# Performance work log

Hardware: AMD Instinct MI355X
Metric: run time of the kernel (lower is better)

The kernel has to match this reference:

```python
import jax, jax.numpy as jnp
import numpy as np

EPS = 1e-5

def _bn_eval(x, gamma, beta, mu, var):
    # channelwise BN (eval mode) on [B,C,N,K]
    inv = gamma / jnp.sqrt(var + EPS)
    return x * inv[None, :, None, None] + (beta - mu * inv)[None, :, None, None]

def _gather_nk(x, idx):
    # x: [B,C,N], idx: [B,N,K] -> [B,C,N,K]
    return jnp.take_along_axis(x[:, :, None, :], idx[:, None, :, :], axis=3)

def setup_inputs() -> dict:
    key = jax.random.key(0)
    ks = jax.random.split(key, 20)
    B, N, K, C = 2, 16384, 16, 128
    s = 0.05
    inp = {
        'coord': jax.random.normal(ks[0], (B, N, 3), jnp.float32),
        'feature_spa': jax.random.normal(ks[1], (B, C, N), jnp.float32),
        'feature_spe': jax.random.normal(ks[2], (B, C, N), jnp.float32),
        'neighbor_indices': jax.random.randint(ks[3], (B, N, K), 0, N),
        'wq': jax.random.normal(ks[4], (C, C), jnp.float32) * s,
        'wk': jax.random.normal(ks[5], (C, C), jnp.float32) * s,
        'wv_w': jax.random.normal(ks[6], (C, C), jnp.float32) * s,
        'wv_b': jax.random.normal(ks[7], (C,), jnp.float32) * s,
        'pos_w1': jax.random.normal(ks[8], (3, 3), jnp.float32) * 0.3,
        'pos_b1': jax.random.normal(ks[9], (3,), jnp.float32) * 0.1,
        'pos_g': jnp.ones((3,), jnp.float32),
        'pos_beta': jnp.zeros((3,), jnp.float32),
        'pos_mu': jnp.zeros((3,), jnp.float32),
        'pos_var': jnp.ones((3,), jnp.float32),
        'pos_w2': jax.random.normal(ks[10], (1, 3), jnp.float32) * 0.3,
        'pos_b2': jax.random.normal(ks[11], (1,), jnp.float32) * 0.1,
        'sc_w1': jax.random.normal(ks[12], (2, 2), jnp.float32) * 0.3,
        'sc_b1': jax.random.normal(ks[13], (2,), jnp.float32) * 0.1,
        'sc_g': jnp.ones((2,), jnp.float32),
        'sc_beta': jnp.zeros((2,), jnp.float32),
        'sc_mu': jnp.zeros((2,), jnp.float32),
        'sc_var': jnp.ones((2,), jnp.float32),
        'sc_w2': jax.random.normal(ks[14], (1, 2), jnp.float32) * 0.3,
        'sc_b2': jax.random.normal(ks[15], (1,), jnp.float32) * 0.1,
    }
    return inp

def reference(coord, feature_spa, feature_spe, neighbor_indices,
              wq, wk, wv_w, wv_b,
              pos_w1, pos_b1, pos_g, pos_beta, pos_mu, pos_var, pos_w2, pos_b2,
              sc_w1, sc_b1, sc_g, sc_beta, sc_mu, sc_var, sc_w2, sc_b2):
    C = feature_spa.shape[1]
    coord_t = jnp.transpose(coord, (0, 2, 1))                      # [B,3,N]
    Q = jnp.einsum('oc,bcn->bon', wq, feature_spa)                 # [B,C,N]
    Kf = jnp.einsum('oc,bcn->bon', wk, feature_spe)
    V = jnp.einsum('oc,bcn->bon', wv_w, feature_spe) + wv_b[None, :, None]
    # positional branch
    neighbor_coord = _gather_nk(coord_t, neighbor_indices)         # [B,3,N,K]
    coord_diff = neighbor_coord - coord_t[:, :, :, None]
    g = jnp.exp(-2.0 * coord_diff ** 2)                            # [B,3,N,K]
    h = jnp.einsum('oc,bcnk->bonk', pos_w1, g) + pos_b1[None, :, None, None]
    h = jax.nn.relu(_bn_eval(h, pos_g, pos_beta, pos_mu, pos_var))
    scores_coord = jnp.einsum('oc,bcnk->bonk', pos_w2, h) + pos_b2[None, :, None, None]  # [B,1,N,K]
    # feature branch
    Kg = _gather_nk(Kf, neighbor_indices)                          # [B,C,N,K]
    Vg = _gather_nk(V, neighbor_indices)                           # [B,C,N,K]
    scores_feat = jnp.einsum('bcn,bcnk->bnk', Q, Kg) / np.sqrt(C)  # [B,N,K]
    scores = jnp.concatenate([scores_coord, scores_feat[:, None]], axis=1)  # [B,2,N,K]
    s = jnp.einsum('oc,bcnk->bonk', sc_w1, scores) + sc_b1[None, :, None, None]
    s = jax.nn.relu(_bn_eval(s, sc_g, sc_beta, sc_mu, sc_var))
    s = jnp.einsum('oc,bcnk->bonk', sc_w2, s) + sc_b2[None, :, None, None]  # [B,1,N,K]
    attn = jax.nn.softmax(s, axis=-1)                              # [B,1,N,K]
    fusion_feat = jnp.sum(attn * Vg, axis=-1)                      # [B,C,N]
    return fusion_feat
```

## Files before the change

kernel.cpp:

```cpp
#include <hip/hip_runtime.h>
#include <cstdint>
#include <cstddef>

#define B_ 2
#define N_ 16384
#define K_ 16
#define C_ 128

typedef __attribute__((ext_vector_type(8))) short  bf16x8;
typedef __attribute__((ext_vector_type(4))) float  f32x4;

__device__ __forceinline__ float bfu_lo(uint32_t w) { return __uint_as_float(w << 16); }
__device__ __forceinline__ float bfu_hi(uint32_t w) { return __uint_as_float(w & 0xffff0000u); }

__device__ __forceinline__ ushort f32_to_bf16_rne(float x) {
    uint32_t u = __float_as_uint(x);
    u += 0x7FFFu + ((u >> 16) & 1u);
    return (ushort)(u >> 16);
}
__device__ __forceinline__ uint32_t pack_bf16x2(float lo, float hi) {
    return (uint32_t)f32_to_bf16_rne(lo) | ((uint32_t)f32_to_bf16_rne(hi) << 16);
}

__device__ __forceinline__ int xswz(int row, int c) {
    return row * 128 + ((((c >> 3) ^ (row & 7)) << 3) | (c & 7));
}

__global__ __launch_bounds__(256) void w_cvt(
    const float* __restrict__ wq, const float* __restrict__ wk,
    const float* __restrict__ wv, ushort* __restrict__ W16all)
{
    const float* src = (blockIdx.y == 0) ? wq : (blockIdx.y == 1 ? wk : wv);
    ushort* dst = W16all + (size_t)blockIdx.y * (C_ * C_);
    const int i = (blockIdx.x * 256 + threadIdx.x) * 8;
    float4 a = *(const float4*)(src + i);
    float4 b4 = *(const float4*)(src + i + 4);
    uint4 pk;
    pk.x = pack_bf16x2(a.x, a.y);
    pk.y = pack_bf16x2(a.z, a.w);
    pk.z = pack_bf16x2(b4.x, b4.y);
    pk.w = pack_bf16x2(b4.z, b4.w);
    *(uint4*)(dst + i) = pk;
}

__global__ __launch_bounds__(512) void qkv_gemm(
    const float* __restrict__ spa, const float* __restrict__ spe,
    const ushort* __restrict__ W16all, const float* __restrict__ wvb,
    ushort* __restrict__ Qt16, ushort* __restrict__ Kt16, ushort* __restrict__ Vt16)
{
    const int nt    = blockIdx.x * 128;
    const int b     = blockIdx.y;
    const int which = blockIdx.z;
    const float*  X   = (which == 0) ? spa : spe;
    const ushort* W16 = W16all + (size_t)which * (C_ * C_);
    ushort* Out       = (which == 0) ? Qt16 : (which == 1 ? Kt16 : Vt16);

    __shared__ ushort xs[128 * 128];
    __shared__ ushort ws[128 * 128];

    const int t    = threadIdx.x;
    const int w    = t >> 6;
    const int lane = t & 63;
    const int l15  = lane & 15;
    const int l4   = lane >> 4;
    const int ow   = (w & 3) * 32;
    const int nw   = (w >> 2) * 64;

    {
        const int r  = t >> 2;
        const int c0 = (t & 3) * 32;
        const uint4* src = (const uint4*)(W16 + r * C_ + c0);
        #pragma unroll
        for (int q = 0; q < 4; ++q) {
            uint4 v = src[q];
            *(uint4*)&ws[xswz(r, c0 + q * 8)] = v;
        }
    }
    {
        const int c  = t >> 2;
        const int nq = (t & 3) * 32;
        const float* xrow = X + ((size_t)b * C_ + c) * N_ + nt + nq;
        #pragma unroll
        for (int q = 0; q < 8; ++q) {
            float4 v = ((const float4*)xrow)[q];
            const int n = nq + q * 4;
            xs[xswz(n + 0, c)] = f32_to_bf16_rne(v.x);
            xs[xswz(n + 1, c)] = f32_to_bf16_rne(v.y);
            xs[xswz(n + 2, c)] = f32_to_bf16_rne(v.z);
            xs[xswz(n + 3, c)] = f32_to_bf16_rne(v.w);
        }
    }
    __syncthreads();

    f32x4 acc[2][4];
    #pragma unroll
    for (int of = 0; of < 2; ++of)
        #pragma unroll
        for (int nf = 0; nf < 4; ++nf)
            acc[of][nf] = (f32x4){0.f, 0.f, 0.f, 0.f};

    #pragma unroll
    for (int kc = 0; kc < 4; ++kc) {
        const int cb = kc * 32 + l4 * 8;
        bf16x8 afr[2];
        #pragma unroll
        for (int of = 0; of < 2; ++of)
            afr[of] = *(__shared__ bf16x8*)&ws[xswz(ow + of * 16 + l15, cb)];
        bf16x8 bfr[4];
        #pragma unroll
        for (int nf = 0; nf < 4; ++nf)
            bfr[nf] = *(__shared__ bf16x8*)&xs[xswz(nw + nf * 16 + l15, cb)];
        #pragma unroll
        for (int of = 0; of < 2; ++of)
            #pragma unroll
            for (int nf = 0; nf < 4; ++nf)
                acc[of][nf] = __builtin_amdgcn_mfma_f32_16x16x32_bf16(
                    afr[of], bfr[nf], acc[of][nf], 0, 0, 0);
    }

    #pragma unroll
    for (int of = 0; of < 2; ++of) {
        const int o0r = ow + of * 16 + l4 * 4;
        float4 bv = make_float4(0.f, 0.f, 0.f, 0.f);
        if (which == 2) bv = *(const float4*)(wvb + o0r);
        #pragma unroll
        for (int nf = 0; nf < 4; ++nf) {
            const int n = nt + nw + nf * 16 + l15;
            uint2 pk;
            pk.x = pack_bf16x2(acc[of][nf][0] + bv.x, acc[of][nf][1] + bv.y);
            pk.y = pack_bf16x2(acc[of][nf][2] + bv.z, acc[of][nf][3] + bv.w);
            *(uint2*)(Out + ((size_t)b * N_ + n) * C_ + o0r) = pk;
        }
    }
}

__global__ __launch_bounds__(256) void attn_fuse(
    const float* __restrict__ coord, const int* __restrict__ nbr,
    const ushort* __restrict__ Qt16, const ushort* __restrict__ Kt16,
    const ushort* __restrict__ Vt16,
    const float* __restrict__ pw1, const float* __restrict__ pb1,
    const float* __restrict__ pg,  const float* __restrict__ pbeta,
    const float* __restrict__ pmu, const float* __restrict__ pvar,
    const float* __restrict__ pw2, const float* __restrict__ pb2,
    const float* __restrict__ sw1, const float* __restrict__ sb1,
    const float* __restrict__ sg,  const float* __restrict__ sbeta,
    const float* __restrict__ smu, const float* __restrict__ svar,
    const float* __restrict__ sw2, const float* __restrict__ sb2,
    float* __restrict__ out)
{
    const int bid  = blockIdx.x;
    const int b    = bid >> 10;
    const int n0   = (bid & 1023) << 4;
    const int t    = threadIdx.x;
    const int w    = t >> 6;
    const int lane = t & 63;
    const int g    = lane >> 2;
    const int sub  = lane & 3;

    __shared__ float qs[16][132];
    __shared__ int   idx_s[16][16];
    __shared__ float cs[16][3];
    __shared__ float ot[128][17];

    {
        const int n = t >> 4, c0 = (t & 15) * 8;
        uint4 qw = *(const uint4*)(Qt16 + ((size_t)(b * N_ + n0 + n)) * C_ + c0);
        qs[n][c0 + 0] = bfu_lo(qw.x); qs[n][c0 + 1] = bfu_hi(qw.x);
        qs[n][c0 + 2] = bfu_lo(qw.y); qs[n][c0 + 3] = bfu_hi(qw.y);
        qs[n][c0 + 4] = bfu_lo(qw.z); qs[n][c0 + 5] = bfu_hi(qw.z);
        qs[n][c0 + 6] = bfu_lo(qw.w); qs[n][c0 + 7] = bfu_hi(qw.w);
        idx_s[t >> 4][t & 15] = nbr[((size_t)(b * N_ + n0 + (t >> 4))) * K_ + (t & 15)];
        if (t < 48) cs[t / 3][t % 3] = coord[((size_t)(b * N_ + n0 + t / 3)) * 3 + (t % 3)];
    }
    __syncthreads();

    float pinv[3], pofs[3], w1r[3][3], w2r[3], pb1r[3];
    #pragma unroll
    for (int o = 0; o < 3; ++o) {
        float inv = pg[o] / sqrtf(pvar[o] + 1e-5f);
        pinv[o] = inv;
        pofs[o] = pbeta[o] - pmu[o] * inv;
        pb1r[o] = pb1[o];
        w2r[o]  = pw2[o];
        #pragma unroll
        for (int i2 = 0; i2 < 3; ++i2) w1r[o][i2] = pw1[o * 3 + i2];
    }
    const float pb2v = pb2[0];
    float sinv[2], sofs[2], sb1r[2];
    #pragma unroll
    for (int o = 0; o < 2; ++o) {
        float inv = sg[o] / sqrtf(svar[o] + 1e-5f);
        sinv[o] = inv;
        sofs[o] = sbeta[o] - smu[o] * inv;
        sb1r[o] = sb1[o];
    }
    const float sw1r[4] = {sw1[0], sw1[1], sw1[2], sw1[3]};
    const float sw2r[2] = {sw2[0], sw2[1]};
    const float sb2v = sb2[0];
    const float inv_sqrtC = 0.088388347648318447f;

    #pragma unroll
    for (int i = 0; i < 4; ++i) {
        const int nl = w * 4 + i;
        const int idxg = idx_s[nl][g];

        const uint4* kp = (const uint4*)(Kt16 + ((size_t)(b * N_ + idxg)) * C_ + sub * 32);
        uint4 kw0 = kp[0], kw1 = kp[1], kw2 = kp[2], kw3 = kp[3];
        uint32_t vv[16];
        #pragma unroll
        for (int k = 0; k < 16; ++k) {
            const int vid = idx_s[nl][k];
            vv[k] = ((const uint32_t*)(Vt16 + ((size_t)(b * N_ + vid)) * C_))[lane];
        }
        const float* ncp = coord + ((size_t)(b * N_ + idxg)) * 3;
        const float nc0 = ncp[0], nc1 = ncp[1], nc2 = ncp[2];

        const float* qrow = &qs[nl][sub * 32];
        float acc = 0.f;
        #pragma unroll
        for (int j = 0; j < 4; ++j) {
            float4 qa = *(const float4*)&qrow[j * 8];
            float4 qb = *(const float4*)&qrow[j * 8 + 4];
            uint4  kwj = (j == 0) ? kw0 : (j == 1) ? kw1 : (j == 2) ? kw2 : kw3;
            acc = fmaf(qa.x, bfu_lo(kwj.x), acc);
            acc = fmaf(qa.y, bfu_hi(kwj.x), acc);
            acc = fmaf(qa.z, bfu_lo(kwj.y), acc);
            acc = fmaf(qa.w, bfu_hi(kwj.y), acc);
            acc = fmaf(qb.x, bfu_lo(kwj.z), acc);
            acc = fmaf(qb.y, bfu_hi(kwj.z), acc);
            acc = fmaf(qb.z, bfu_lo(kwj.w), acc);
            acc = fmaf(qb.w, bfu_hi(kwj.w), acc);
        }
        acc += __shfl_xor(acc, 1);
        acc += __shfl_xor(acc, 2);
        const float sfeat = acc * inv_sqrtC;

        float d0 = nc0 - cs[nl][0], d1 = nc1 - cs[nl][1], d2 = nc2 - cs[nl][2];
        float g0 = expf(-2.f * d0 * d0);
        float g1 = expf(-2.f * d1 * d1);
        float g2 = expf(-2.f * d2 * d2);
        float h0 = fmaf(w1r[0][0], g0, fmaf(w1r[0][1], g1, fmaf(w1r[0][2], g2, pb1r[0])));
        float h1 = fmaf(w1r[1][0], g0, fmaf(w1r[1][1], g1, fmaf(w1r[1][2], g2, pb1r[1])));
        float h2 = fmaf(w1r[2][0], g0, fmaf(w1r[2][1], g1, fmaf(w1r[2][2], g2, pb1r[2])));
        h0 = fmaxf(fmaf(h0, pinv[0], pofs[0]), 0.f);
        h1 = fmaxf(fmaf(h1, pinv[1], pofs[1]), 0.f);
        h2 = fmaxf(fmaf(h2, pinv[2], pofs[2]), 0.f);
        const float scoord = fmaf(w2r[0], h0, fmaf(w2r[1], h1, fmaf(w2r[2], h2, pb2v)));

        float t0 = fmaf(sw1r[0], scoord, fmaf(sw1r[1], sfeat, sb1r[0]));
        t0 = fmaxf(fmaf(t0, sinv[0], sofs[0]), 0.f);
        float t1 = fmaf(sw1r[2], scoord, fmaf(sw1r[3], sfeat, sb1r[1]));
        t1 = fmaxf(fmaf(t1, sinv[1], sofs[1]), 0.f);
        float s = fmaf(sw2r[0], t0, fmaf(sw2r[1], t1, sb2v));

        float m = s;
        m = fmaxf(m, __shfl_xor(m, 4));
        m = fmaxf(m, __shfl_xor(m, 8));
        m = fmaxf(m, __shfl_xor(m, 16));
        m = fmaxf(m, __shfl_xor(m, 32));
        float e = expf(s - m);
        float den = e;
        den += __shfl_xor(den, 4);
        den += __shfl_xor(den, 8);
        den += __shfl_xor(den, 16);
        den += __shfl_xor(den, 32);
        const float attn = e / den;

        float a0 = 0.f, a1 = 0.f;
        #pragma unroll
        for (int k = 0; k < 16; ++k) {
            const float ak = __shfl(attn, k << 2);
            a0 = fmaf(ak, bfu_lo(vv[k]), a0);
            a1 = fmaf(ak, bfu_hi(vv[k]), a1);
        }
        ot[2 * lane][nl]     = a0;
        ot[2 * lane + 1][nl] = a1;
    }
    __syncthreads();

    {
        const int col = t & 15;
        const int r0  = (t >> 4) * 8;
        #pragma unroll
        for (int r = 0; r < 8; ++r)
            out[((size_t)(b * C_ + r0 + r)) * N_ + n0 + col] = ot[r0 + r][col];
    }
}

extern "C" void kernel_launch(void* const* d_in, const int* in_sizes, int n_in,
                              void* d_out, int out_size, void* d_ws, size_t ws_size,
                              hipStream_t stream) {
    const float* coord = (const float*)d_in[0];
    const float* spa   = (const float*)d_in[1];
    const float* spe   = (const float*)d_in[2];
    const int*   nbr   = (const int*)  d_in[3];
    const float* wq    = (const float*)d_in[4];
    const float* wk    = (const float*)d_in[5];
    const float* wv    = (const float*)d_in[6];
    const float* wvb   = (const float*)d_in[7];
    const float* pw1   = (const float*)d_in[8];
    const float* pb1   = (const float*)d_in[9];
    const float* pg    = (const float*)d_in[10];
    const float* pbeta = (const float*)d_in[11];
    const float* pmu   = (const float*)d_in[12];
    const float* pvar  = (const float*)d_in[13];
    const float* pw2   = (const float*)d_in[14];
    const float* pb2   = (const float*)d_in[15];
    const float* sw1   = (const float*)d_in[16];
    const float* sb1   = (const float*)d_in[17];
    const float* sg    = (const float*)d_in[18];
    const float* sbeta = (const float*)d_in[19];
    const float* smu   = (const float*)d_in[20];
    const float* svar  = (const float*)d_in[21];
    const float* sw2   = (const float*)d_in[22];
    const float* sb2   = (const float*)d_in[23];
    float* out = (float*)d_out;

    ushort* Qt16  = (ushort*)d_ws;
    ushort* Kt16  = Qt16 + (size_t)B_ * N_ * C_;
    ushort* Vt16  = Kt16 + (size_t)B_ * N_ * C_;
    ushort* W16all = Vt16 + (size_t)B_ * N_ * C_;

    w_cvt<<<dim3(8, 3), 256, 0, stream>>>(wq, wk, wv, W16all);

    qkv_gemm<<<dim3(N_ / 128, B_, 3), 512, 0, stream>>>(
        spa, spe, W16all, wvb, Qt16, Kt16, Vt16);

    attn_fuse<<<dim3(B_ * N_ / 16), 256, 0, stream>>>(
        coord, nbr, Qt16, Kt16, Vt16,
        pw1, pb1, pg, pbeta, pmu, pvar, pw2, pb2,
        sw1, sb1, sg, sbeta, smu, svar, sw2, sb2,
        out);
}
```

Measured before the change: 173.5 us.

## Store K projection as FP8 e5m2 and fold weight conversion into GEMM

The K projection is now written as 8-bit e5m2 values instead of bf16, which halves the bytes fetched per gathered neighbour key in the attention kernel. The key dot product decodes the bytes through fp16 in software. Separately, the standalone weight-conversion kernel is removed and each GEMM block converts its fp32 weights to bf16 while loading them, saving one launch at the cost of redundant conversion work per block. The 2-bit mantissa adds noticeable error to the feature scores and may threaten accuracy tolerance.

```diff
diff --git a/kernel.cpp b/kernel.cpp
--- a/kernel.cpp
+++ b/kernel.cpp
@@ -22,38 +22,33 @@
     return (uint32_t)f32_to_bf16_rne(lo) | ((uint32_t)f32_to_bf16_rne(hi) << 16);
 }
 
+__device__ __forceinline__ uint32_t e5m2_enc(float x) {
+    union { _Float16 h; ushort u; } cv;
+    cv.h = (_Float16)x;
+    ushort h = (ushort)(cv.u + 0x7Fu + ((cv.u >> 8) & 1u));
+    return (uint32_t)(h >> 8) & 0xFFu;
+}
+__device__ __forceinline__ float e5m2_dec(uint32_t byteval) {
+    union { _Float16 h; ushort u; } cv;
+    cv.u = (ushort)(byteval << 8);
+    return (float)cv.h;
+}
+
 __device__ __forceinline__ int xswz(int row, int c) {
     return row * 128 + ((((c >> 3) ^ (row & 7)) << 3) | (c & 7));
 }
 
-__global__ __launch_bounds__(256) void w_cvt(
-    const float* __restrict__ wq, const float* __restrict__ wk,
-    const float* __restrict__ wv, ushort* __restrict__ W16all)
-{
-    const float* src = (blockIdx.y == 0) ? wq : (blockIdx.y == 1 ? wk : wv);
-    ushort* dst = W16all + (size_t)blockIdx.y * (C_ * C_);
-    const int i = (blockIdx.x * 256 + threadIdx.x) * 8;
-    float4 a = *(const float4*)(src + i);
-    float4 b4 = *(const float4*)(src + i + 4);
-    uint4 pk;
-    pk.x = pack_bf16x2(a.x, a.y);
-    pk.y = pack_bf16x2(a.z, a.w);
-    pk.z = pack_bf16x2(b4.x, b4.y);
-    pk.w = pack_bf16x2(b4.z, b4.w);
-    *(uint4*)(dst + i) = pk;
-}
-
 __global__ __launch_bounds__(512) void qkv_gemm(
     const float* __restrict__ spa, const float* __restrict__ spe,
-    const ushort* __restrict__ W16all, const float* __restrict__ wvb,
-    ushort* __restrict__ Qt16, ushort* __restrict__ Kt16, ushort* __restrict__ Vt16)
+    const float* __restrict__ wq, const float* __restrict__ wk,
+    const float* __restrict__ wv, const float* __restrict__ wvb,
+    ushort* __restrict__ Qt16, uint8_t* __restrict__ Kt8, ushort* __restrict__ Vt16)
 {
     const int nt    = blockIdx.x * 128;
     const int b     = blockIdx.y;
     const int which = blockIdx.z;
-    const float*  X   = (which == 0) ? spa : spe;
-    const ushort* W16 = W16all + (size_t)which * (C_ * C_);
-    ushort* Out       = (which == 0) ? Qt16 : (which == 1 ? Kt16 : Vt16);
+    const float* X = (which == 0) ? spa : spe;
+    const float* W = (which == 0) ? wq : (which == 1 ? wk : wv);
 
     __shared__ ushort xs[128 * 128];
     __shared__ ushort ws[128 * 128];
@@ -69,11 +64,17 @@
     {
         const int r  = t >> 2;
         const int c0 = (t & 3) * 32;
-        const uint4* src = (const uint4*)(W16 + r * C_ + c0);
+        const float* srcw = W + r * C_ + c0;
         #pragma unroll
         for (int q = 0; q < 4; ++q) {
-            uint4 v = src[q];
-            *(uint4*)&ws[xswz(r, c0 + q * 8)] = v;
+            float4 a  = *(const float4*)(srcw + q * 8);
+            float4 b4 = *(const float4*)(srcw + q * 8 + 4);
+            uint4 pk;
+            pk.x = pack_bf16x2(a.x, a.y);
+            pk.y = pack_bf16x2(a.z, a.w);
+            pk.z = pack_bf16x2(b4.x, b4.y);
+            pk.w = pack_bf16x2(b4.z, b4.w);
+            *(uint4*)&ws[xswz(r, c0 + q * 8)] = pk;
         }
     }
     {
@@ -121,22 +122,35 @@
     #pragma unroll
     for (int of = 0; of < 2; ++of) {
         const int o0r = ow + of * 16 + l4 * 4;
-        float4 bv = make_float4(0.f, 0.f, 0.f, 0.f);
-        if (which == 2) bv = *(const float4*)(wvb + o0r);
-        #pragma unroll
-        for (int nf = 0; nf < 4; ++nf) {
-            const int n = nt + nw + nf * 16 + l15;
-            uint2 pk;
-            pk.x = pack_bf16x2(acc[of][nf][0] + bv.x, acc[of][nf][1] + bv.y);
-            pk.y = pack_bf16x2(acc[of][nf][2] + bv.z, acc[of][nf][3] + bv.w);
-            *(uint2*)(Out + ((size_t)b * N_ + n) * C_ + o0r) = pk;
+        if (which == 1) {
+            #pragma unroll
+            for (int nf = 0; nf < 4; ++nf) {
+                const int n = nt + nw + nf * 16 + l15;
+                uint32_t w8 = e5m2_enc(acc[of][nf][0])
+                            | (e5m2_enc(acc[of][nf][1]) << 8)
+                            | (e5m2_enc(acc[of][nf][2]) << 16)
+                            | (e5m2_enc(acc[of][nf][3]) << 24);
+                *(uint32_t*)(Kt8 + ((size_t)b * N_ + n) * C_ + o0r) = w8;
+            }
+        } else {
+            ushort* Out = (which == 0) ? Qt16 : Vt16;
+            float4 bv = make_float4(0.f, 0.f, 0.f, 0.f);
+            if (which == 2) bv = *(const float4*)(wvb + o0r);
+            #pragma unroll
+            for (int nf = 0; nf < 4; ++nf) {
+                const int n = nt + nw + nf * 16 + l15;
+                uint2 pk;
+                pk.x = pack_bf16x2(acc[of][nf][0] + bv.x, acc[of][nf][1] + bv.y);
+                pk.y = pack_bf16x2(acc[of][nf][2] + bv.z, acc[of][nf][3] + bv.w);
+                *(uint2*)(Out + ((size_t)b * N_ + n) * C_ + o0r) = pk;
+            }
         }
     }
 }
 
 __global__ __launch_bounds__(256) void attn_fuse(
     const float* __restrict__ coord, const int* __restrict__ nbr,
-    const ushort* __restrict__ Qt16, const ushort* __restrict__ Kt16,
+    const ushort* __restrict__ Qt16, const uint8_t* __restrict__ Kt8,
     const ushort* __restrict__ Vt16,
     const float* __restrict__ pw1, const float* __restrict__ pb1,
     const float* __restrict__ pg,  const float* __restrict__ pbeta,
@@ -204,8 +218,8 @@
         const int nl = w * 4 + i;
         const int idxg = idx_s[nl][g];
 
-        const uint4* kp = (const uint4*)(Kt16 + ((size_t)(b * N_ + idxg)) * C_ + sub * 32);
-        uint4 kw0 = kp[0], kw1 = kp[1], kw2 = kp[2], kw3 = kp[3];
+        const uint4* kp = (const uint4*)(Kt8 + ((size_t)(b * N_ + idxg)) * C_ + sub * 32);
+        uint4 ka = kp[0], kb = kp[1];
         uint32_t vv[16];
         #pragma unroll
         for (int k = 0; k < 16; ++k) {
@@ -217,19 +231,16 @@
 
         const float* qrow = &qs[nl][sub * 32];
         float acc = 0.f;
-        #pragma unroll
-        for (int j = 0; j < 4; ++j) {
-            float4 qa = *(const float4*)&qrow[j * 8];
-            float4 qb = *(const float4*)&qrow[j * 8 + 4];
-            uint4  kwj = (j == 0) ? kw0 : (j == 1) ? kw1 : (j == 2) ? kw2 : kw3;
-            acc = fmaf(qa.x, bfu_lo(kwj.x), acc);
-            acc = fmaf(qa.y, bfu_hi(kwj.x), acc);
-            acc = fmaf(qa.z, bfu_lo(kwj.y), acc);
-            acc = fmaf(qa.w, bfu_hi(kwj.y), acc);
-            acc = fmaf(qb.x, bfu_lo(kwj.z), acc);
-            acc = fmaf(qb.y, bfu_hi(kwj.z), acc);
-            acc = fmaf(qb.z, bfu_lo(kwj.w), acc);
-            acc = fmaf(qb.w, bfu_hi(kwj.w), acc);
+        {
+            const uint32_t wds[8] = {ka.x, ka.y, ka.z, ka.w, kb.x, kb.y, kb.z, kb.w};
+            #pragma unroll
+            for (int j = 0; j < 8; ++j) {
+                const uint32_t ww = wds[j];
+                acc = fmaf(qrow[j * 4 + 0], e5m2_dec(ww & 0xffu), acc);
+                acc = fmaf(qrow[j * 4 + 1], e5m2_dec((ww >> 8) & 0xffu), acc);
+                acc = fmaf(qrow[j * 4 + 2], e5m2_dec((ww >> 16) & 0xffu), acc);
+                acc = fmaf(qrow[j * 4 + 3], e5m2_dec(ww >> 24), acc);
+            }
         }
         acc += __shfl_xor(acc, 1);
         acc += __shfl_xor(acc, 2);
@@ -316,18 +327,15 @@
     const float* sb2   = (const float*)d_in[23];
     float* out = (float*)d_out;
 
-    ushort* Qt16  = (ushort*)d_ws;
-    ushort* Kt16  = Qt16 + (size_t)B_ * N_ * C_;
-    ushort* Vt16  = Kt16 + (size_t)B_ * N_ * C_;
-    ushort* W16all = Vt16 + (size_t)B_ * N_ * C_;
-
-    w_cvt<<<dim3(8, 3), 256, 0, stream>>>(wq, wk, wv, W16all);
+    ushort*  Qt16 = (ushort*)d_ws;
+    ushort*  Vt16 = Qt16 + (size_t)B_ * N_ * C_;
+    uint8_t* Kt8  = (uint8_t*)(Vt16 + (size_t)B_ * N_ * C_);
 
     qkv_gemm<<<dim3(N_ / 128, B_, 3), 512, 0, stream>>>(
-        spa, spe, W16all, wvb, Qt16, Kt16, Vt16);
+        spa, spe, wq, wk, wv, wvb, Qt16, Kt8, Vt16);
 
     attn_fuse<<<dim3(B_ * N_ / 16), 256, 0, stream>>>(
-        coord, nbr, Qt16, Kt16, Vt16,
+        coord, nbr, Qt16, Kt8, Vt16,
         pw1, pb1, pg, pbeta, pmu, pvar, pw2, pb2,
         sw1, sb1, sg, sbeta, smu, svar, sw2, sb2,
         out);
```

After: 168.8 us. 1.03x faster.
